# Kernel optimization log

Measured on AMD Instinct MI355X. Metric: run time of the kernel, lower is better.

Reference implementation:

```python
import jax, jax.numpy as jnp
import numpy as np

N = 1_000_000   # total nodes
B = 1024        # number of graphs
H = 64          # node feature dim / LSTM hidden
STEPS = 5       # Set2Set processing steps
PROJ = 128      # projection_dim


def setup_inputs() -> dict:
    key = jax.random.key(0)
    ks = jax.random.split(key, 12)
    x = jax.random.normal(ks[0], (N, H), dtype=jnp.float32)
    batch = jnp.sort(jax.random.randint(ks[1], (N,), 0, B)).astype(jnp.int64)
    s = 1.0 / np.sqrt(H)
    # torch.nn.LSTM(input_size=2H, hidden_size=H), gate order i,f,g,o
    W_ih = jax.random.uniform(ks[2], (4 * H, 2 * H), minval=-s, maxval=s, dtype=jnp.float32)
    W_hh = jax.random.uniform(ks[3], (4 * H, H), minval=-s, maxval=s, dtype=jnp.float32)
    b_ih = jax.random.uniform(ks[4], (4 * H,), minval=-s, maxval=s, dtype=jnp.float32)
    b_hh = jax.random.uniform(ks[5], (4 * H,), minval=-s, maxval=s, dtype=jnp.float32)
    s1 = 1.0 / np.sqrt(2 * H)
    W1 = jax.random.uniform(ks[6], (256, 2 * H), minval=-s1, maxval=s1, dtype=jnp.float32)
    b1 = jax.random.uniform(ks[7], (256,), minval=-s1, maxval=s1, dtype=jnp.float32)
    s2 = 1.0 / np.sqrt(256)
    W2 = jax.random.uniform(ks[8], (PROJ, 256), minval=-s2, maxval=s2, dtype=jnp.float32)
    b2 = jax.random.uniform(ks[9], (PROJ,), minval=-s2, maxval=s2, dtype=jnp.float32)
    return {"x": x, "batch": batch, "W_ih": W_ih, "W_hh": W_hh, "b_ih": b_ih,
            "b_hh": b_hh, "W1": W1, "b1": b1, "W2": W2, "b2": b2}


def _set2set(x, batch, W_ih, W_hh, b_ih, b_hh):
    q_star = jnp.zeros((B, 2 * H), x.dtype)
    h = jnp.zeros((B, H), x.dtype)
    c = jnp.zeros((B, H), x.dtype)
    for _ in range(STEPS):
        gates = q_star @ W_ih.T + b_ih + h @ W_hh.T + b_hh
        i, f, g, o = jnp.split(gates, 4, axis=-1)
        i = jax.nn.sigmoid(i); f = jax.nn.sigmoid(f)
        g = jnp.tanh(g); o = jax.nn.sigmoid(o)
        c = f * c + i * g
        h = o * jnp.tanh(c)
        q = h  # [B, H]
        # segment-wise attention over ragged node sets
        e = jnp.sum(x * q[batch], axis=-1)                         # [N]
        emax = jax.ops.segment_max(e, batch, num_segments=B)       # [B]
        a = jnp.exp(e - emax[batch])
        denom = jax.ops.segment_sum(a, batch, num_segments=B)
        a = a / jnp.maximum(denom, 1e-16)[batch]
        r = jax.ops.segment_sum(a[:, None] * x, batch, num_segments=B)  # [B, H]
        q_star = jnp.concatenate([q, r], axis=-1)
    return q_star


def reference(x, batch, W_ih, W_hh, b_ih, b_hh, W1, b1, W2, b2):
    out = _set2set(x, batch, W_ih, W_hh, b_ih, b_hh)   # [B, 2H]
    out = out @ W1.T + b1                               # [B, 256]
    out = jax.nn.relu(out) @ W2.T + b2                  # [B, PROJ]
    return out
```

## Files before the change

### kernel.cpp

```cpp
#include <hip/hip_runtime.h>
#include <float.h>
#include <math.h>

#define NB 1024
#define HD 64
#define NSTEPS 5
#define SPLIT 4

__device__ __forceinline__ float sigmoidf_(float x) {
    return 1.0f / (1.0f + __expf(-x));
}

__global__ void seg_bounds_kernel(const int* __restrict__ batch,
                                  int* __restrict__ seg_start, int n) {
    int i = blockIdx.x * blockDim.x + threadIdx.x;
    if (i >= n) return;
    int b = batch[i];
    if (i == 0) {
        for (int j = 0; j <= b; ++j) seg_start[j] = 0;
    } else {
        int pb = batch[i - 1];
        for (int j = pb + 1; j <= b; ++j) seg_start[j] = i;
    }
    if (i == n - 1) {
        for (int j = b + 1; j <= NB; ++j) seg_start[j] = n;
    }
}

__global__ void lstm_kernel(const float* __restrict__ W_ih,
                            const float* __restrict__ W_hh,
                            const float* __restrict__ b_ih,
                            const float* __restrict__ b_hh,
                            const float* __restrict__ pm,
                            const float* __restrict__ ps,
                            const float* __restrict__ pr,
                            float* __restrict__ h,
                            float* __restrict__ c,
                            int first) {
    const int G = 8;
    int g0 = blockIdx.x * G;
    __shared__ float s_qs[G][128];
    __shared__ float s_gates[G][256];
    int tid = threadIdx.x;

    if (!first) {
        for (int idx = tid; idx < G * 64; idx += 256) {
            int g = idx >> 6, k = idx & 63;
            s_qs[g][k] = h[(g0 + g) * 64 + k];
        }
        for (int idx = tid; idx < G * 64; idx += 256) {
            int g = idx >> 6, k = idx & 63;
            int b = g0 + g;
            float m0 = pm[b * SPLIT + 0], m1 = pm[b * SPLIT + 1];
            float m2 = pm[b * SPLIT + 2], m3 = pm[b * SPLIT + 3];
            float M = fmaxf(fmaxf(m0, m1), fmaxf(m2, m3));
            float w0 = __expf(m0 - M), w1 = __expf(m1 - M);
            float w2 = __expf(m2 - M), w3 = __expf(m3 - M);
            float S = ps[b * SPLIT + 0] * w0 + ps[b * SPLIT + 1] * w1
                    + ps[b * SPLIT + 2] * w2 + ps[b * SPLIT + 3] * w3;
            float rf = pr[(b * SPLIT + 0) * 64 + k] * w0
                     + pr[(b * SPLIT + 1) * 64 + k] * w1
                     + pr[(b * SPLIT + 2) * 64 + k] * w2
                     + pr[(b * SPLIT + 3) * 64 + k] * w3;
            s_qs[g][64 + k] = rf / fmaxf(S, 1e-16f);
        }
        __syncthreads();
    }

    int j = tid;
    float acc[G];
    float bias = b_ih[j] + b_hh[j];
#pragma unroll
    for (int g = 0; g < G; ++g) acc[g] = bias;

    if (!first) {
        const float4* wih = (const float4*)(W_ih + j * 128);
#pragma unroll 4
        for (int k4 = 0; k4 < 32; ++k4) {
            float4 w = wih[k4];
#pragma unroll
            for (int g = 0; g < G; ++g) {
                acc[g] = fmaf(w.x, s_qs[g][k4 * 4 + 0], acc[g]);
                acc[g] = fmaf(w.y, s_qs[g][k4 * 4 + 1], acc[g]);
                acc[g] = fmaf(w.z, s_qs[g][k4 * 4 + 2], acc[g]);
                acc[g] = fmaf(w.w, s_qs[g][k4 * 4 + 3], acc[g]);
            }
        }
        const float4* whh = (const float4*)(W_hh + j * 64);
#pragma unroll 4
        for (int k4 = 0; k4 < 16; ++k4) {
            float4 w = whh[k4];
#pragma unroll
            for (int g = 0; g < G; ++g) {
                acc[g] = fmaf(w.x, s_qs[g][k4 * 4 + 0], acc[g]);
                acc[g] = fmaf(w.y, s_qs[g][k4 * 4 + 1], acc[g]);
                acc[g] = fmaf(w.z, s_qs[g][k4 * 4 + 2], acc[g]);
                acc[g] = fmaf(w.w, s_qs[g][k4 * 4 + 3], acc[g]);
            }
        }
    }
#pragma unroll
    for (int g = 0; g < G; ++g) s_gates[g][j] = acc[g];
    __syncthreads();

    for (int idx = tid; idx < G * 64; idx += 256) {
        int g = idx >> 6, jj = idx & 63;
        int gb = g0 + g;
        float ig = sigmoidf_(s_gates[g][jj]);
        float fg = sigmoidf_(s_gates[g][jj + 64]);
        float gg = tanhf(s_gates[g][jj + 128]);
        float og = sigmoidf_(s_gates[g][jj + 192]);
        float cprev = first ? 0.0f : c[gb * 64 + jj];
        float cn = fmaf(fg, cprev, ig * gg);
        float hn = og * tanhf(cn);
        c[gb * 64 + jj] = cn;
        h[gb * 64 + jj] = hn;
    }
}

__global__ __launch_bounds__(256) void attn_kernel(const float* __restrict__ x,
                                                   const int* __restrict__ seg_start,
                                                   const float* __restrict__ h,
                                                   float* __restrict__ pm,
                                                   float* __restrict__ ps,
                                                   float* __restrict__ pr) {
    int bs = blockIdx.x;
    int b = bs >> 2;
    int slice = bs & (SPLIT - 1);
    int s0 = seg_start[b], e0 = seg_start[b + 1];
    int len = e0 - s0;
    int s = s0 + (int)(((long long)len * slice) >> 2);
    int e = s0 + (int)(((long long)len * (slice + 1)) >> 2);

    int tid = threadIdx.x;
    int lane = tid & 63;
    int wave = tid >> 6;
    int fc = lane & 15;
    int grp = lane >> 4;

    float4 q4 = *(const float4*)(h + b * 64 + fc * 4);

    float m = -FLT_MAX, sum = 0.0f;
    float4 r4 = make_float4(0.0f, 0.0f, 0.0f, 0.0f);

    const int maxidx4 = e * 16 - 1;
    for (int base = s + wave * 16; base < e; base += 64) {
#pragma unroll
        for (int t = 0; t < 4; ++t) {
            int node = base + t * 4 + grp;
            int idx4 = base * 16 + t * 64 + lane;
            idx4 = min(idx4, maxidx4);
            float4 xv = *(const float4*)(x + (size_t)idx4 * 4);

            float d = xv.x * q4.x;
            d = fmaf(xv.y, q4.y, d);
            d = fmaf(xv.z, q4.z, d);
            d = fmaf(xv.w, q4.w, d);
            d += __shfl_xor(d, 1);
            d += __shfl_xor(d, 2);
            d += __shfl_xor(d, 4);
            d += __shfl_xor(d, 8);

            bool valid = node < e;
            float eeff = valid ? d : -FLT_MAX;
            float nm = fmaxf(m, eeff);
            float sc = __expf(m - nm);
            float w = valid ? __expf(eeff - nm) : 0.0f;
            sum = fmaf(sum, sc, w);
            r4.x = fmaf(r4.x, sc, w * xv.x);
            r4.y = fmaf(r4.y, sc, w * xv.y);
            r4.z = fmaf(r4.z, sc, w * xv.z);
            r4.w = fmaf(r4.w, sc, w * xv.w);
            m = nm;
        }
    }

#pragma unroll
    for (int off = 16; off < 64; off <<= 1) {
        float om = __shfl_xor(m, off);
        float os = __shfl_xor(sum, off);
        float ox = __shfl_xor(r4.x, off);
        float oy = __shfl_xor(r4.y, off);
        float oz = __shfl_xor(r4.z, off);
        float ow = __shfl_xor(r4.w, off);
        float nm = fmaxf(m, om);
        float s1 = __expf(m - nm);
        float s2 = __expf(om - nm);
        sum = sum * s1 + os * s2;
        r4.x = r4.x * s1 + ox * s2;
        r4.y = r4.y * s1 + oy * s2;
        r4.z = r4.z * s1 + oz * s2;
        r4.w = r4.w * s1 + ow * s2;
        m = nm;
    }

    __shared__ float lm[4], ls[4], lr[4][64];
    if (lane < 16) {
        if (lane == 0) { lm[wave] = m; ls[wave] = sum; }
        *(float4*)&lr[wave][lane * 4] = r4;
    }
    __syncthreads();
    if (tid < 64) {
        float M = fmaxf(fmaxf(lm[0], lm[1]), fmaxf(lm[2], lm[3]));
        float w0 = __expf(lm[0] - M), w1 = __expf(lm[1] - M);
        float w2 = __expf(lm[2] - M), w3 = __expf(lm[3] - M);
        float S = ls[0] * w0 + ls[1] * w1 + ls[2] * w2 + ls[3] * w3;
        float rf = lr[0][tid] * w0 + lr[1][tid] * w1 + lr[2][tid] * w2 + lr[3][tid] * w3;
        if (tid == 0) { pm[bs] = M; ps[bs] = S; }
        pr[bs * 64 + tid] = rf;
    }
}

__global__ void mlp_kernel(const float* __restrict__ h,
                           const float* __restrict__ pm,
                           const float* __restrict__ ps,
                           const float* __restrict__ pr,
                           const float* __restrict__ W1,
                           const float* __restrict__ b1,
                           const float* __restrict__ W2,
                           const float* __restrict__ b2,
                           float* __restrict__ out) {
    int b = blockIdx.x;
    __shared__ float qs[128];
    __shared__ float hid[256];
    int tid = threadIdx.x;
    if (tid < 64) {
        qs[tid] = h[b * 64 + tid];
    } else if (tid < 128) {
        int k = tid - 64;
        float m0 = pm[b * SPLIT + 0], m1 = pm[b * SPLIT + 1];
        float m2 = pm[b * SPLIT + 2], m3 = pm[b * SPLIT + 3];
        float M = fmaxf(fmaxf(m0, m1), fmaxf(m2, m3));
        float w0 = __expf(m0 - M), w1 = __expf(m1 - M);
        float w2 = __expf(m2 - M), w3 = __expf(m3 - M);
        float S = ps[b * SPLIT + 0] * w0 + ps[b * SPLIT + 1] * w1
                + ps[b * SPLIT + 2] * w2 + ps[b * SPLIT + 3] * w3;
        float rf = pr[(b * SPLIT + 0) * 64 + k] * w0
                 + pr[(b * SPLIT + 1) * 64 + k] * w1
                 + pr[(b * SPLIT + 2) * 64 + k] * w2
                 + pr[(b * SPLIT + 3) * 64 + k] * w3;
        qs[tid] = rf / fmaxf(S, 1e-16f);
    }
    __syncthreads();
    float acc = b1[tid];
    const float4* w = (const float4*)(W1 + tid * 128);
#pragma unroll 4
    for (int k4 = 0; k4 < 32; ++k4) {
        float4 ww = w[k4];
        acc = fmaf(ww.x, qs[k4 * 4 + 0], acc);
        acc = fmaf(ww.y, qs[k4 * 4 + 1], acc);
        acc = fmaf(ww.z, qs[k4 * 4 + 2], acc);
        acc = fmaf(ww.w, qs[k4 * 4 + 3], acc);
    }
    hid[tid] = fmaxf(acc, 0.0f);
    __syncthreads();
    if (tid < 128) {
        float acc2 = b2[tid];
        const float4* w2 = (const float4*)(W2 + tid * 256);
#pragma unroll 4
        for (int k4 = 0; k4 < 64; ++k4) {
            float4 ww = w2[k4];
            acc2 = fmaf(ww.x, hid[k4 * 4 + 0], acc2);
            acc2 = fmaf(ww.y, hid[k4 * 4 + 1], acc2);
            acc2 = fmaf(ww.z, hid[k4 * 4 + 2], acc2);
            acc2 = fmaf(ww.w, hid[k4 * 4 + 3], acc2);
        }
        out[b * 128 + tid] = acc2;
    }
}

extern "C" void kernel_launch(void* const* d_in, const int* in_sizes, int n_in,
                              void* d_out, int out_size, void* d_ws, size_t ws_size,
                              hipStream_t stream) {
    const float* x    = (const float*)d_in[0];
    const int*   batch= (const int*)d_in[1];
    const float* W_ih = (const float*)d_in[2];
    const float* W_hh = (const float*)d_in[3];
    const float* b_ih = (const float*)d_in[4];
    const float* b_hh = (const float*)d_in[5];
    const float* W1   = (const float*)d_in[6];
    const float* b1   = (const float*)d_in[7];
    const float* W2   = (const float*)d_in[8];
    const float* b2   = (const float*)d_in[9];
    float* out = (float*)d_out;
    const int N = in_sizes[1];

    float* h   = (float*)d_ws;
    float* c   = h + NB * 64;
    int*   seg = (int*)(c + NB * 64);
    float* pm  = (float*)(seg + NB + 8);
    float* ps  = pm + NB * SPLIT;
    float* pr  = ps + NB * SPLIT;

    seg_bounds_kernel<<<(N + 255) / 256, 256, 0, stream>>>(batch, seg, N);

    for (int step = 0; step < NSTEPS; ++step) {
        lstm_kernel<<<NB / 8, 256, 0, stream>>>(W_ih, W_hh, b_ih, b_hh,
                                                pm, ps, pr, h, c, step == 0 ? 1 : 0);
        attn_kernel<<<NB * SPLIT, 256, 0, stream>>>(x, seg, h, pm, ps, pr);
    }
    mlp_kernel<<<NB, 256, 0, stream>>>(h, pm, ps, pr, W1, b1, W2, b2, out);
}
```

Before: 615.8 us.

## Fuse LSTM, attention steps and MLP into one per-graph persistent kernel

Replaces the per-step LSTM and split attention launches plus the final MLP with one kernel that gives each graph a 512-thread block running all five Set2Set steps and the projection in shared memory. Node features are streamed through double-buffered LDS with async global-to-LDS loads and explicit vmcnt waits, so loads overlap compute. This removes eleven launches, the global partial-softmax buffers and their merge. It drops the four-way split of each segment, leaving only 1024 blocks, and every step re-reads x (about 256 MB per step) with less parallelism per segment.

```diff
diff --git a/kernel.cpp b/kernel.cpp
--- a/kernel.cpp
+++ b/kernel.cpp
@@ -5,7 +5,6 @@
 #define NB 1024
 #define HD 64
 #define NSTEPS 5
-#define SPLIT 4
 
 __device__ __forceinline__ float sigmoidf_(float x) {
     return 1.0f / (1.0f + __expf(-x));
@@ -27,277 +26,252 @@
     }
 }
 
-__global__ void lstm_kernel(const float* __restrict__ W_ih,
-                            const float* __restrict__ W_hh,
-                            const float* __restrict__ b_ih,
-                            const float* __restrict__ b_hh,
-                            const float* __restrict__ pm,
-                            const float* __restrict__ ps,
-                            const float* __restrict__ pr,
-                            float* __restrict__ h,
-                            float* __restrict__ c,
-                            int first) {
-    const int G = 8;
-    int g0 = blockIdx.x * G;
-    __shared__ float s_qs[G][128];
-    __shared__ float s_gates[G][256];
-    int tid = threadIdx.x;
-
-    if (!first) {
-        for (int idx = tid; idx < G * 64; idx += 256) {
-            int g = idx >> 6, k = idx & 63;
-            s_qs[g][k] = h[(g0 + g) * 64 + k];
-        }
-        for (int idx = tid; idx < G * 64; idx += 256) {
-            int g = idx >> 6, k = idx & 63;
-            int b = g0 + g;
-            float m0 = pm[b * SPLIT + 0], m1 = pm[b * SPLIT + 1];
-            float m2 = pm[b * SPLIT + 2], m3 = pm[b * SPLIT + 3];
-            float M = fmaxf(fmaxf(m0, m1), fmaxf(m2, m3));
-            float w0 = __expf(m0 - M), w1 = __expf(m1 - M);
-            float w2 = __expf(m2 - M), w3 = __expf(m3 - M);
-            float S = ps[b * SPLIT + 0] * w0 + ps[b * SPLIT + 1] * w1
-                    + ps[b * SPLIT + 2] * w2 + ps[b * SPLIT + 3] * w3;
-            float rf = pr[(b * SPLIT + 0) * 64 + k] * w0
-                     + pr[(b * SPLIT + 1) * 64 + k] * w1
-                     + pr[(b * SPLIT + 2) * 64 + k] * w2
-                     + pr[(b * SPLIT + 3) * 64 + k] * w3;
-            s_qs[g][64 + k] = rf / fmaxf(S, 1e-16f);
-        }
-        __syncthreads();
-    }
-
-    int j = tid;
-    float acc[G];
-    float bias = b_ih[j] + b_hh[j];
-#pragma unroll
-    for (int g = 0; g < G; ++g) acc[g] = bias;
-
-    if (!first) {
-        const float4* wih = (const float4*)(W_ih + j * 128);
-#pragma unroll 4
-        for (int k4 = 0; k4 < 32; ++k4) {
-            float4 w = wih[k4];
-#pragma unroll
-            for (int g = 0; g < G; ++g) {
-                acc[g] = fmaf(w.x, s_qs[g][k4 * 4 + 0], acc[g]);
-                acc[g] = fmaf(w.y, s_qs[g][k4 * 4 + 1], acc[g]);
-                acc[g] = fmaf(w.z, s_qs[g][k4 * 4 + 2], acc[g]);
-                acc[g] = fmaf(w.w, s_qs[g][k4 * 4 + 3], acc[g]);
-            }
-        }
-        const float4* whh = (const float4*)(W_hh + j * 64);
-#pragma unroll 4
-        for (int k4 = 0; k4 < 16; ++k4) {
-            float4 w = whh[k4];
-#pragma unroll
-            for (int g = 0; g < G; ++g) {
-                acc[g] = fmaf(w.x, s_qs[g][k4 * 4 + 0], acc[g]);
-                acc[g] = fmaf(w.y, s_qs[g][k4 * 4 + 1], acc[g]);
-                acc[g] = fmaf(w.z, s_qs[g][k4 * 4 + 2], acc[g]);
-                acc[g] = fmaf(w.w, s_qs[g][k4 * 4 + 3], acc[g]);
-            }
-        }
-    }
-#pragma unroll
-    for (int g = 0; g < G; ++g) s_gates[g][j] = acc[g];
+__device__ __forceinline__ void async_ld16(const float* g, float* l) {
+    __builtin_amdgcn_global_load_lds(
+        (const __attribute__((address_space(1))) void*)g,
+        (__attribute__((address_space(3))) void*)l, 16, 0, 0);
+}
+
+__global__ __launch_bounds__(512, 4) void set2set_fused_kernel(
+    const float* __restrict__ x,
+    const int* __restrict__ seg,
+    const float* __restrict__ W_ih,
+    const float* __restrict__ W_hh,
+    const float* __restrict__ b_ih,
+    const float* __restrict__ b_hh,
+    const float* __restrict__ W1,
+    const float* __restrict__ b1,
+    const float* __restrict__ W2,
+    const float* __restrict__ b2,
+    float* __restrict__ out)
+{
+    __shared__ __align__(16) float sbuf[8][2][16 * HD];
+    __shared__ __align__(16) float hs[HD], cs[HD], rs[HD];
+    __shared__ __align__(16) float gates[256], gpart[256];
+    __shared__ __align__(16) float lr[8][HD];
+    __shared__ float lm[8], ls[8];
+
+    const int b = blockIdx.x;
+    const int tid = threadIdx.x;
+    const int lane = tid & 63;
+    const int wv = tid >> 6;
+    const int fc = lane & 15;
+    const int grp = lane >> 4;
+
+    const int s0 = seg[b], e0 = seg[b + 1];
+    const int len = e0 - s0;
+    const int ntiles = (len + 15) >> 4;
+    const int maxidx4 = e0 * 16 - 1;
+
+    if (tid < HD) { hs[tid] = 0.0f; cs[tid] = 0.0f; rs[tid] = 0.0f; }
     __syncthreads();
 
-    for (int idx = tid; idx < G * 64; idx += 256) {
-        int g = idx >> 6, jj = idx & 63;
-        int gb = g0 + g;
-        float ig = sigmoidf_(s_gates[g][jj]);
-        float fg = sigmoidf_(s_gates[g][jj + 64]);
-        float gg = tanhf(s_gates[g][jj + 128]);
-        float og = sigmoidf_(s_gates[g][jj + 192]);
-        float cprev = first ? 0.0f : c[gb * 64 + jj];
-        float cn = fmaf(fg, cprev, ig * gg);
-        float hn = og * tanhf(cn);
-        c[gb * 64 + jj] = cn;
-        h[gb * 64 + jj] = hn;
-    }
-}
-
-__global__ __launch_bounds__(256) void attn_kernel(const float* __restrict__ x,
-                                                   const int* __restrict__ seg_start,
-                                                   const float* __restrict__ h,
-                                                   float* __restrict__ pm,
-                                                   float* __restrict__ ps,
-                                                   float* __restrict__ pr) {
-    int bs = blockIdx.x;
-    int b = bs >> 2;
-    int slice = bs & (SPLIT - 1);
-    int s0 = seg_start[b], e0 = seg_start[b + 1];
-    int len = e0 - s0;
-    int s = s0 + (int)(((long long)len * slice) >> 2);
-    int e = s0 + (int)(((long long)len * (slice + 1)) >> 2);
-
-    int tid = threadIdx.x;
-    int lane = tid & 63;
-    int wave = tid >> 6;
-    int fc = lane & 15;
-    int grp = lane >> 4;
-
-    float4 q4 = *(const float4*)(h + b * 64 + fc * 4);
-
-    float m = -FLT_MAX, sum = 0.0f;
-    float4 r4 = make_float4(0.0f, 0.0f, 0.0f, 0.0f);
-
-    const int maxidx4 = e * 16 - 1;
-    for (int base = s + wave * 16; base < e; base += 64) {
-#pragma unroll
-        for (int t = 0; t < 4; ++t) {
-            int node = base + t * 4 + grp;
-            int idx4 = base * 16 + t * 64 + lane;
-            idx4 = min(idx4, maxidx4);
-            float4 xv = *(const float4*)(x + (size_t)idx4 * 4);
-
-            float d = xv.x * q4.x;
-            d = fmaf(xv.y, q4.y, d);
-            d = fmaf(xv.z, q4.z, d);
-            d = fmaf(xv.w, q4.w, d);
-            d += __shfl_xor(d, 1);
-            d += __shfl_xor(d, 2);
-            d += __shfl_xor(d, 4);
-            d += __shfl_xor(d, 8);
-
-            bool valid = node < e;
-            float eeff = valid ? d : -FLT_MAX;
-            float nm = fmaxf(m, eeff);
-            float sc = __expf(m - nm);
-            float w = valid ? __expf(eeff - nm) : 0.0f;
-            sum = fmaf(sum, sc, w);
-            r4.x = fmaf(r4.x, sc, w * xv.x);
-            r4.y = fmaf(r4.y, sc, w * xv.y);
-            r4.z = fmaf(r4.z, sc, w * xv.z);
-            r4.w = fmaf(r4.w, sc, w * xv.w);
+    for (int step = 0; step < NSTEPS; ++step) {
+        if (wv < ntiles) {
+            const int tb4 = (s0 + wv * 16) * 16;
+            float* dst = &sbuf[wv][0][0];
+#pragma unroll
+            for (int i = 0; i < 4; ++i) {
+                int g4 = min(tb4 + i * 64 + lane, maxidx4);
+                async_ld16(x + (size_t)g4 * 4, dst + i * 256);
+            }
+        }
+
+        if (step == 0) {
+            if (tid < 256) gates[tid] = b_ih[tid] + b_hh[tid];
+        } else {
+            float acc = 0.0f;
+            if (tid < 256) {
+                acc = b_ih[tid] + b_hh[tid];
+                const float4* w = (const float4*)(W_ih + tid * 128);
+                const float4* hq = (const float4*)hs;
+                const float4* rq = (const float4*)rs;
+#pragma unroll
+                for (int k = 0; k < 16; ++k) {
+                    float4 ww = w[k]; float4 v = hq[k];
+                    acc = fmaf(ww.x, v.x, acc); acc = fmaf(ww.y, v.y, acc);
+                    acc = fmaf(ww.z, v.z, acc); acc = fmaf(ww.w, v.w, acc);
+                }
+#pragma unroll
+                for (int k = 0; k < 16; ++k) {
+                    float4 ww = w[16 + k]; float4 v = rq[k];
+                    acc = fmaf(ww.x, v.x, acc); acc = fmaf(ww.y, v.y, acc);
+                    acc = fmaf(ww.z, v.z, acc); acc = fmaf(ww.w, v.w, acc);
+                }
+            } else {
+                int j = tid - 256;
+                float a2 = 0.0f;
+                const float4* w = (const float4*)(W_hh + j * 64);
+                const float4* hq = (const float4*)hs;
+#pragma unroll
+                for (int k = 0; k < 16; ++k) {
+                    float4 ww = w[k]; float4 v = hq[k];
+                    a2 = fmaf(ww.x, v.x, a2); a2 = fmaf(ww.y, v.y, a2);
+                    a2 = fmaf(ww.z, v.z, a2); a2 = fmaf(ww.w, v.w, a2);
+                }
+                gpart[j] = a2;
+            }
+            __syncthreads();
+            if (tid < 256) gates[tid] = acc + gpart[tid];
+        }
+        __syncthreads();
+
+        if (tid < HD) {
+            float ig = sigmoidf_(gates[tid]);
+            float fg = sigmoidf_(gates[tid + 64]);
+            float gg = tanhf(gates[tid + 128]);
+            float og = sigmoidf_(gates[tid + 192]);
+            float cp = (step == 0) ? 0.0f : cs[tid];
+            float cn = fmaf(fg, cp, ig * gg);
+            cs[tid] = cn;
+            hs[tid] = og * tanhf(cn);
+        }
+        __syncthreads();
+
+        float4 q4 = *(const float4*)(hs + fc * 4);
+        float m = -FLT_MAX, sum = 0.0f;
+        float4 r4 = make_float4(0.0f, 0.0f, 0.0f, 0.0f);
+
+        int cur = 0;
+        for (int t = wv; t < ntiles; t += 8) {
+            __builtin_amdgcn_sched_barrier(0);
+            int nxt = t + 8;
+            if (nxt < ntiles) {
+                const int tb4 = (s0 + nxt * 16) * 16;
+                float* dst = &sbuf[wv][cur ^ 1][0];
+#pragma unroll
+                for (int i = 0; i < 4; ++i) {
+                    int g4 = min(tb4 + i * 64 + lane, maxidx4);
+                    async_ld16(x + (size_t)g4 * 4, dst + i * 256);
+                }
+                asm volatile("s_waitcnt vmcnt(4)" ::: "memory");
+            } else {
+                asm volatile("s_waitcnt vmcnt(0)" ::: "memory");
+            }
+            __builtin_amdgcn_sched_barrier(0);
+
+            const float* buf = &sbuf[wv][cur][0];
+            const int nbase = t * 16;
+#pragma unroll
+            for (int u = 0; u < 4; ++u) {
+                int nl = u * 4 + grp;
+                float4 xv = *(const float4*)(buf + nl * 64 + fc * 4);
+                float d = xv.x * q4.x;
+                d = fmaf(xv.y, q4.y, d);
+                d = fmaf(xv.z, q4.z, d);
+                d = fmaf(xv.w, q4.w, d);
+                d += __shfl_xor(d, 1);
+                d += __shfl_xor(d, 2);
+                d += __shfl_xor(d, 4);
+                d += __shfl_xor(d, 8);
+                bool valid = (nbase + nl) < len;
+                float eeff = valid ? d : -FLT_MAX;
+                float nm = fmaxf(m, eeff);
+                float sc = __expf(m - nm);
+                float w = valid ? __expf(eeff - nm) : 0.0f;
+                sum = fmaf(sum, sc, w);
+                r4.x = fmaf(r4.x, sc, w * xv.x);
+                r4.y = fmaf(r4.y, sc, w * xv.y);
+                r4.z = fmaf(r4.z, sc, w * xv.z);
+                r4.w = fmaf(r4.w, sc, w * xv.w);
+                m = nm;
+            }
+            cur ^= 1;
+        }
+
+#pragma unroll
+        for (int off = 16; off < 64; off <<= 1) {
+            float om = __shfl_xor(m, off);
+            float os = __shfl_xor(sum, off);
+            float ox = __shfl_xor(r4.x, off);
+            float oy = __shfl_xor(r4.y, off);
+            float oz = __shfl_xor(r4.z, off);
+            float ow = __shfl_xor(r4.w, off);
+            float nm = fmaxf(m, om);
+            float s1 = __expf(m - nm);
+            float s2 = __expf(om - nm);
+            sum = sum * s1 + os * s2;
+            r4.x = r4.x * s1 + ox * s2;
+            r4.y = r4.y * s1 + oy * s2;
+            r4.z = r4.z * s1 + oz * s2;
+            r4.w = r4.w * s1 + ow * s2;
             m = nm;
         }
-    }
-
-#pragma unroll
-    for (int off = 16; off < 64; off <<= 1) {
-        float om = __shfl_xor(m, off);
-        float os = __shfl_xor(sum, off);
-        float ox = __shfl_xor(r4.x, off);
-        float oy = __shfl_xor(r4.y, off);
-        float oz = __shfl_xor(r4.z, off);
-        float ow = __shfl_xor(r4.w, off);
-        float nm = fmaxf(m, om);
-        float s1 = __expf(m - nm);
-        float s2 = __expf(om - nm);
-        sum = sum * s1 + os * s2;
-        r4.x = r4.x * s1 + ox * s2;
-        r4.y = r4.y * s1 + oy * s2;
-        r4.z = r4.z * s1 + oz * s2;
-        r4.w = r4.w * s1 + ow * s2;
-        m = nm;
-    }
-
-    __shared__ float lm[4], ls[4], lr[4][64];
-    if (lane < 16) {
-        if (lane == 0) { lm[wave] = m; ls[wave] = sum; }
-        *(float4*)&lr[wave][lane * 4] = r4;
-    }
-    __syncthreads();
-    if (tid < 64) {
-        float M = fmaxf(fmaxf(lm[0], lm[1]), fmaxf(lm[2], lm[3]));
-        float w0 = __expf(lm[0] - M), w1 = __expf(lm[1] - M);
-        float w2 = __expf(lm[2] - M), w3 = __expf(lm[3] - M);
-        float S = ls[0] * w0 + ls[1] * w1 + ls[2] * w2 + ls[3] * w3;
-        float rf = lr[0][tid] * w0 + lr[1][tid] * w1 + lr[2][tid] * w2 + lr[3][tid] * w3;
-        if (tid == 0) { pm[bs] = M; ps[bs] = S; }
-        pr[bs * 64 + tid] = rf;
-    }
-}
-
-__global__ void mlp_kernel(const float* __restrict__ h,
-                           const float* __restrict__ pm,
-                           const float* __restrict__ ps,
-                           const float* __restrict__ pr,
-                           const float* __restrict__ W1,
-                           const float* __restrict__ b1,
-                           const float* __restrict__ W2,
-                           const float* __restrict__ b2,
-                           float* __restrict__ out) {
-    int b = blockIdx.x;
-    __shared__ float qs[128];
-    __shared__ float hid[256];
-    int tid = threadIdx.x;
-    if (tid < 64) {
-        qs[tid] = h[b * 64 + tid];
-    } else if (tid < 128) {
-        int k = tid - 64;
-        float m0 = pm[b * SPLIT + 0], m1 = pm[b * SPLIT + 1];
-        float m2 = pm[b * SPLIT + 2], m3 = pm[b * SPLIT + 3];
-        float M = fmaxf(fmaxf(m0, m1), fmaxf(m2, m3));
-        float w0 = __expf(m0 - M), w1 = __expf(m1 - M);
-        float w2 = __expf(m2 - M), w3 = __expf(m3 - M);
-        float S = ps[b * SPLIT + 0] * w0 + ps[b * SPLIT + 1] * w1
-                + ps[b * SPLIT + 2] * w2 + ps[b * SPLIT + 3] * w3;
-        float rf = pr[(b * SPLIT + 0) * 64 + k] * w0
-                 + pr[(b * SPLIT + 1) * 64 + k] * w1
-                 + pr[(b * SPLIT + 2) * 64 + k] * w2
-                 + pr[(b * SPLIT + 3) * 64 + k] * w3;
-        qs[tid] = rf / fmaxf(S, 1e-16f);
-    }
-    __syncthreads();
-    float acc = b1[tid];
-    const float4* w = (const float4*)(W1 + tid * 128);
-#pragma unroll 4
-    for (int k4 = 0; k4 < 32; ++k4) {
-        float4 ww = w[k4];
-        acc = fmaf(ww.x, qs[k4 * 4 + 0], acc);
-        acc = fmaf(ww.y, qs[k4 * 4 + 1], acc);
-        acc = fmaf(ww.z, qs[k4 * 4 + 2], acc);
-        acc = fmaf(ww.w, qs[k4 * 4 + 3], acc);
-    }
-    hid[tid] = fmaxf(acc, 0.0f);
+        if (lane < 16) {
+            if (lane == 0) { lm[wv] = m; ls[wv] = sum; }
+            *(float4*)&lr[wv][lane * 4] = r4;
+        }
+        __syncthreads();
+
+        if (tid < HD) {
+            float M = lm[0];
+#pragma unroll
+            for (int w = 1; w < 8; ++w) M = fmaxf(M, lm[w]);
+            float S = 0.0f, rf = 0.0f;
+#pragma unroll
+            for (int w = 0; w < 8; ++w) {
+                float ww = __expf(lm[w] - M);
+                S = fmaf(ls[w], ww, S);
+                rf = fmaf(lr[w][tid], ww, rf);
+            }
+            rs[tid] = rf / fmaxf(S, 1e-16f);
+        }
+        __syncthreads();
+    }
+
+    if (tid < 256) {
+        float acc = b1[tid];
+        const float4* w = (const float4*)(W1 + tid * 128);
+        const float4* hq = (const float4*)hs;
+        const float4* rq = (const float4*)rs;
+#pragma unroll
+        for (int k = 0; k < 16; ++k) {
+            float4 ww = w[k]; float4 v = hq[k];
+            acc = fmaf(ww.x, v.x, acc); acc = fmaf(ww.y, v.y, acc);
+            acc = fmaf(ww.z, v.z, acc); acc = fmaf(ww.w, v.w, acc);
+        }
+#pragma unroll
+        for (int k = 0; k < 16; ++k) {
+            float4 ww = w[16 + k]; float4 v = rq[k];
+            acc = fmaf(ww.x, v.x, acc); acc = fmaf(ww.y, v.y, acc);
+            acc = fmaf(ww.z, v.z, acc); acc = fmaf(ww.w, v.w, acc);
+        }
+        gates[tid] = fmaxf(acc, 0.0f);
+    }
     __syncthreads();
     if (tid < 128) {
-        float acc2 = b2[tid];
-        const float4* w2 = (const float4*)(W2 + tid * 256);
-#pragma unroll 4
-        for (int k4 = 0; k4 < 64; ++k4) {
-            float4 ww = w2[k4];
-            acc2 = fmaf(ww.x, hid[k4 * 4 + 0], acc2);
-            acc2 = fmaf(ww.y, hid[k4 * 4 + 1], acc2);
-            acc2 = fmaf(ww.z, hid[k4 * 4 + 2], acc2);
-            acc2 = fmaf(ww.w, hid[k4 * 4 + 3], acc2);
-        }
-        out[b * 128 + tid] = acc2;
+        float acc = b2[tid];
+        const float4* w = (const float4*)(W2 + tid * 256);
+        const float4* hq = (const float4*)gates;
+#pragma unroll 8
+        for (int k = 0; k < 64; ++k) {
+            float4 ww = w[k]; float4 v = hq[k];
+            acc = fmaf(ww.x, v.x, acc); acc = fmaf(ww.y, v.y, acc);
+            acc = fmaf(ww.z, v.z, acc); acc = fmaf(ww.w, v.w, acc);
+        }
+        out[b * 128 + tid] = acc;
     }
 }
 
 extern "C" void kernel_launch(void* const* d_in, const int* in_sizes, int n_in,
                               void* d_out, int out_size, void* d_ws, size_t ws_size,
                               hipStream_t stream) {
-    const float* x    = (const float*)d_in[0];
-    const int*   batch= (const int*)d_in[1];
-    const float* W_ih = (const float*)d_in[2];
-    const float* W_hh = (const float*)d_in[3];
-    const float* b_ih = (const float*)d_in[4];
-    const float* b_hh = (const float*)d_in[5];
-    const float* W1   = (const float*)d_in[6];
-    const float* b1   = (const float*)d_in[7];
-    const float* W2   = (const float*)d_in[8];
-    const float* b2   = (const float*)d_in[9];
+    const float* x     = (const float*)d_in[0];
+    const int*   batch = (const int*)d_in[1];
+    const float* W_ih  = (const float*)d_in[2];
+    const float* W_hh  = (const float*)d_in[3];
+    const float* b_ih  = (const float*)d_in[4];
+    const float* b_hh  = (const float*)d_in[5];
+    const float* W1    = (const float*)d_in[6];
+    const float* b1    = (const float*)d_in[7];
+    const float* W2    = (const float*)d_in[8];
+    const float* b2    = (const float*)d_in[9];
     float* out = (float*)d_out;
     const int N = in_sizes[1];
 
-    float* h   = (float*)d_ws;
-    float* c   = h + NB * 64;
-    int*   seg = (int*)(c + NB * 64);
-    float* pm  = (float*)(seg + NB + 8);
-    float* ps  = pm + NB * SPLIT;
-    float* pr  = ps + NB * SPLIT;
+    int* seg = (int*)d_ws;
 
     seg_bounds_kernel<<<(N + 255) / 256, 256, 0, stream>>>(batch, seg, N);
-
-    for (int step = 0; step < NSTEPS; ++step) {
-        lstm_kernel<<<NB / 8, 256, 0, stream>>>(W_ih, W_hh, b_ih, b_hh,
-                                                pm, ps, pr, h, c, step == 0 ? 1 : 0);
-        attn_kernel<<<NB * SPLIT, 256, 0, stream>>>(x, seg, h, pm, ps, pr);
-    }
-    mlp_kernel<<<NB, 256, 0, stream>>>(h, pm, ps, pr, W1, b1, W2, b2, out);
-}
+    set2set_fused_kernel<<<NB, 512, 0, stream>>>(x, seg, W_ih, W_hh, b_ih, b_hh,
+                                                 W1, b1, W2, b2, out);
+}
```

Measured after the change: 561.9 us. 8.7% less time.
